# Performance work log

Measured on AMD Instinct MI355X. Metric: run time of the kernel, lower is better.

Reference implementation:

```python
import jax, jax.numpy as jnp
import numpy as np

DIM = 1536
HEADS = 12
HD = DIM // HEADS           # 128
C = HD // 2                 # 64 rotary pairs per head
B = 1
F_, H_, W_ = 16, 16, 16
S = F_ * H_ * W_            # 4096
MAXPOS = 1024
EPS = 1e-6
SPLITS = (C - 2 * (C // 3), C // 3, C // 3)  # (22, 21, 21)


def setup_inputs() -> dict:
    key = jax.random.key(0)
    ks = jax.random.split(key, 8)
    std = 0.02
    x = jax.random.normal(ks[0], (B, S, DIM), jnp.float32)
    seq_lens = jnp.full((B,), S, dtype=jnp.int32)
    grid_sizes = jnp.tile(jnp.array([[F_, H_, W_]], jnp.int32), (B, 1))
    # rotary angle table: per split, theta_j = pos / 10000^(j/size)
    angs = []
    pos = jnp.arange(MAXPOS, dtype=jnp.float32)
    for sz in SPLITS:
        inv = 1.0 / (10000.0 ** (jnp.arange(sz, dtype=jnp.float32) / sz))
        angs.append(jnp.outer(pos, inv))
    freqs = jnp.concatenate(angs, axis=1)  # [MAXPOS, C]
    return {
        "x": x,
        "seq_lens": seq_lens,
        "grid_sizes": grid_sizes,
        "freqs": freqs,
        "wq": jax.random.normal(ks[1], (DIM, DIM), jnp.float32) * std,
        "bq": jnp.zeros((DIM,), jnp.float32),
        "wk": jax.random.normal(ks[2], (DIM, DIM), jnp.float32) * std,
        "bk": jnp.zeros((DIM,), jnp.float32),
        "wv": jax.random.normal(ks[3], (DIM, DIM), jnp.float32) * std,
        "bv": jnp.zeros((DIM,), jnp.float32),
        "wo": jax.random.normal(ks[4], (DIM, DIM), jnp.float32) * std,
        "bo": jnp.zeros((DIM,), jnp.float32),
        "gq": jnp.ones((DIM,), jnp.float32),
        "gk": jnp.ones((DIM,), jnp.float32),
    }


def _rms_norm(x, g):
    # x * rsqrt(mean(x^2) + eps) * g  (WanRMSNorm)
    var = jnp.mean(jnp.square(x), axis=-1, keepdims=True)
    return x * jax.lax.rsqrt(var + EPS) * g


def _rope(x, freqs, f, h, w):
    # x: [b, s, n, hd]; freqs: [MAXPOS, C] angles; grid (f,h,w), s = f*h*w
    fa = freqs[:f, : SPLITS[0]]
    ha = freqs[:h, SPLITS[0] : SPLITS[0] + SPLITS[1]]
    wa = freqs[:w, SPLITS[0] + SPLITS[1] :]
    ang = jnp.concatenate(
        [
            jnp.broadcast_to(fa[:, None, None, :], (f, h, w, SPLITS[0])),
            jnp.broadcast_to(ha[None, :, None, :], (f, h, w, SPLITS[1])),
            jnp.broadcast_to(wa[None, None, :, :], (f, h, w, SPLITS[2])),
        ],
        axis=-1,
    ).reshape(f * h * w, 1, C)  # [s, 1, C] broadcasts over heads
    cos, sin = jnp.cos(ang), jnp.sin(ang)
    xr = x[..., 0::2]  # real parts of complex pairs
    xi = x[..., 1::2]  # imag parts
    out_r = xr * cos - xi * sin
    out_i = xr * sin + xi * cos
    return jnp.stack([out_r, out_i], axis=-1).reshape(x.shape)


def reference(x, seq_lens, grid_sizes, freqs, wq, bq, wk, bk, wv, bv, wo, bo, gq, gk):
    b, s = x.shape[:2]
    q = _rms_norm(x @ wq.T + bq, gq).reshape(b, s, HEADS, HD)
    k = _rms_norm(x @ wk.T + bk, gk).reshape(b, s, HEADS, HD)
    v = (x @ wv.T + bv).reshape(b, s, HEADS, HD)
    # all samples share the same grid (static for jit)
    q = _rope(q, freqs, F_, H_, W_)
    k = _rope(k, freqs, F_, H_, W_)
    scale = 1.0 / np.sqrt(HD)
    scores = jnp.einsum("bqnd,bknd->bnqk", q, k) * scale  # [b, n, s, s]
    k_pos = jnp.arange(s)
    mask = k_pos[None, None, None, :] < seq_lens[:, None, None, None]
    scores = scores + jnp.where(mask, 0.0, -1e9)
    attn = jax.nn.softmax(scores, axis=-1)
    out = jnp.einsum("bnqk,bknd->bqnd", attn, v).reshape(b, s, DIM)
    return out @ wo.T + bo
```

## Files before the change

kernel.cpp:

```cpp
#include <hip/hip_runtime.h>
#include <hip/hip_bf16.h>

#define DIM   1536
#define HEADS 12
#define HD    128
#define SEQ   4096
#define QSCALE 0.08838834764831845f
#define LOG2E 1.44269504088896f

typedef __attribute__((ext_vector_type(8))) short short8;
typedef __attribute__((ext_vector_type(4))) float f32x4;
typedef __attribute__((ext_vector_type(16))) float f32x16;

__device__ __forceinline__ unsigned short f2bf(float f) {
    __hip_bfloat16 h = __float2bfloat16(f);
    return *reinterpret_cast<unsigned short*>(&h);
}
__device__ __forceinline__ float bf2f(unsigned short u) {
    return __uint_as_float(((unsigned int)u) << 16);
}
__device__ __forceinline__ void async_cp16(void* lds, const void* g) {
    __builtin_amdgcn_global_load_lds(
        (const __attribute__((address_space(1))) unsigned int*)g,
        (__attribute__((address_space(3))) unsigned int*)lds, 16, 0, 0);
}

__global__ __launch_bounds__(256) void convert_bf16(
    const float* __restrict__ src, __hip_bfloat16* __restrict__ dst, int n8)
{
    const int i = blockIdx.x * 256 + threadIdx.x;
    if (i >= n8) return;
    const float4 a = *reinterpret_cast<const float4*>(src + (size_t)i * 8);
    const float4 b = *reinterpret_cast<const float4*>(src + (size_t)i * 8 + 4);
    uint4 o;
    o.x = (unsigned int)f2bf(a.x) | ((unsigned int)f2bf(a.y) << 16);
    o.y = (unsigned int)f2bf(a.z) | ((unsigned int)f2bf(a.w) << 16);
    o.z = (unsigned int)f2bf(b.x) | ((unsigned int)f2bf(b.y) << 16);
    o.w = (unsigned int)f2bf(b.z) | ((unsigned int)f2bf(b.w) << 16);
    *reinterpret_cast<uint4*>(dst + (size_t)i * 8) = o;
}

__global__ __launch_bounds__(256) void gemm_qkv(
    const __hip_bfloat16* __restrict__ xb,
    const __hip_bfloat16* __restrict__ wqb, const float* __restrict__ bq,
    const __hip_bfloat16* __restrict__ wkb, const float* __restrict__ bk,
    const __hip_bfloat16* __restrict__ wvb, const float* __restrict__ bv,
    __hip_bfloat16* __restrict__ yq, __hip_bfloat16* __restrict__ yk,
    __hip_bfloat16* __restrict__ vrow)
{
    __shared__ __align__(16) short As[128][32];
    __shared__ __align__(16) short Bs[128][32];
    const int z  = blockIdx.z;
    const __hip_bfloat16* W = (z == 0) ? wqb : (z == 1) ? wkb : wvb;
    const float* bias = (z == 0) ? bq : (z == 1) ? bk : bv;
    __hip_bfloat16* outp = (z == 0) ? yq : (z == 1) ? yk : vrow;
    const int bm0 = blockIdx.x * 128;
    const int bn0 = blockIdx.y * 128;
    const int tid  = threadIdx.x;
    const int lane = tid & 63;
    const int wid  = tid >> 6;
    const int wm = (wid >> 1) * 64;
    const int wn = (wid & 1)  * 64;
    const int fr = lane & 15;
    const int fc = (lane >> 4) * 8;
    const int srow = tid >> 2;
    const int scol = (tid & 3) * 8;

    f32x4 acc[4][4] = {};

    for (int kt = 0; kt < DIM; kt += 32) {
        #pragma unroll
        for (int i = 0; i < 2; i++) {
            async_cp16(&As[i * 64 + ((tid >> 6) << 4)][0],
                       xb + (size_t)(bm0 + i * 64 + srow) * DIM + kt + scol);
            async_cp16(&Bs[i * 64 + ((tid >> 6) << 4)][0],
                       W + (size_t)(bn0 + i * 64 + srow) * DIM + kt + scol);
        }
        __syncthreads();
        short8 af[4], bf8[4];
        #pragma unroll
        for (int m = 0; m < 4; m++) af[m]  = *reinterpret_cast<const short8*>(&As[wm + m * 16 + fr][fc]);
        #pragma unroll
        for (int n = 0; n < 4; n++) bf8[n] = *reinterpret_cast<const short8*>(&Bs[wn + n * 16 + fr][fc]);
        #pragma unroll
        for (int m = 0; m < 4; m++)
            #pragma unroll
            for (int n = 0; n < 4; n++)
                acc[m][n] = __builtin_amdgcn_mfma_f32_16x16x32_bf16(af[m], bf8[n], acc[m][n], 0, 0, 0);
        __syncthreads();
    }

    const int crow0 = bm0 + wm + (lane >> 4) * 4;
    const int ccol0 = bn0 + wn + fr;
    #pragma unroll
    for (int n = 0; n < 4; n++) {
        const int col = ccol0 + n * 16;
        const float bb = bias[col];
        #pragma unroll
        for (int m = 0; m < 4; m++)
            #pragma unroll
            for (int r = 0; r < 4; r++)
                outp[(size_t)(crow0 + m * 16 + r) * DIM + col] =
                    __float2bfloat16(acc[m][n][r] + bb);
    }
}

__global__ __launch_bounds__(256) void rmsnorm_rope(
    __hip_bfloat16* __restrict__ yq, __hip_bfloat16* __restrict__ yk,
    const float* __restrict__ gq, const float* __restrict__ gk,
    const float* __restrict__ freqs)
{
    const int s = blockIdx.x;
    const int z = blockIdx.y;
    __hip_bfloat16* y = z ? yk : yq;
    const float* g = z ? gk : gq;
    const int t = threadIdx.x;

    float xr[3], xi[3];
    float ss = 0.f;
    #pragma unroll
    for (int i = 0; i < 3; i++) {
        const int p = t + i * 256;
        const unsigned int uu = *reinterpret_cast<const unsigned int*>(&y[(size_t)s * DIM + 2 * p]);
        xr[i] = bf2f((unsigned short)(uu & 0xffffu));
        xi[i] = bf2f((unsigned short)(uu >> 16));
        ss += xr[i] * xr[i] + xi[i] * xi[i];
    }
    #pragma unroll
    for (int m = 1; m < 64; m <<= 1) ss += __shfl_xor(ss, m, 64);
    __shared__ float red[4];
    if ((t & 63) == 0) red[t >> 6] = ss;
    __syncthreads();
    const float sum = red[0] + red[1] + red[2] + red[3];
    const float rs = rsqrtf(sum * (1.0f / DIM) + 1e-6f);
    const int f = s >> 8, hh = (s >> 4) & 15, ww = s & 15;
    const float osc = z ? 1.0f : QSCALE;
    #pragma unroll
    for (int i = 0; i < 3; i++) {
        const int p = t + i * 256;
        const int cc = p & 63;
        const int pos = (cc < 22) ? f : (cc < 43) ? hh : ww;
        const float ang = freqs[pos * 64 + cc];
        float sn, cs;
        sincosf(ang, &sn, &cs);
        const float a = xr[i] * rs * g[2 * p];
        const float b = xi[i] * rs * g[2 * p + 1];
        const unsigned int pk = (unsigned int)f2bf((a * cs - b * sn) * osc)
                              | ((unsigned int)f2bf((a * sn + b * cs) * osc) << 16);
        *reinterpret_cast<unsigned int*>(&y[(size_t)s * DIM + 2 * p]) = pk;
    }
}

__global__ __launch_bounds__(256) void transpose_v(
    const __hip_bfloat16* __restrict__ vrow,
    __hip_bfloat16* __restrict__ vT)
{
    __shared__ __align__(16) short tile[64][72];
    const int s0 = blockIdx.x * 64;
    const int c0 = blockIdx.y * 64;
    const int t = threadIdx.x;
    #pragma unroll
    for (int i = 0; i < 2; i++) {
        const int ch = t + i * 256;
        const int r = ch >> 3, cc = (ch & 7) * 8;
        *reinterpret_cast<int4*>(&tile[r][cc]) =
            *reinterpret_cast<const int4*>(&vrow[(size_t)(s0 + r) * DIM + c0 + cc]);
    }
    __syncthreads();
    #pragma unroll
    for (int i = 0; i < 2; i++) {
        const int ch = t + i * 256;
        const int c = ch & 63, sc = (ch >> 6) * 8;
        unsigned int w0 = (unsigned short)tile[sc + 0][c] | ((unsigned int)(unsigned short)tile[sc + 1][c] << 16);
        unsigned int w1 = (unsigned short)tile[sc + 2][c] | ((unsigned int)(unsigned short)tile[sc + 3][c] << 16);
        unsigned int w2 = (unsigned short)tile[sc + 4][c] | ((unsigned int)(unsigned short)tile[sc + 5][c] << 16);
        unsigned int w3 = (unsigned short)tile[sc + 6][c] | ((unsigned int)(unsigned short)tile[sc + 7][c] << 16);
        int4 val;
        val.x = (int)w0; val.y = (int)w1; val.z = (int)w2; val.w = (int)w3;
        *reinterpret_cast<int4*>(&vT[(size_t)(c0 + c) * SEQ + s0 + sc]) = val;
    }
}

__global__ __launch_bounds__(256, 2) void flash_attn(
    const __hip_bfloat16* __restrict__ qb,
    const __hip_bfloat16* __restrict__ kb,
    const __hip_bfloat16* __restrict__ vT,
    const int* __restrict__ seq_lens,
    __hip_bfloat16* __restrict__ attno)
{
    __shared__ __align__(16) short Ks[2][64][128];
    __shared__ __align__(16) short Vs[3][128][64];
    const int qt = blockIdx.x;
    const int h  = blockIdx.y;
    const int tid = threadIdx.x;
    const int lane = tid & 63;
    const int w = tid >> 6;
    const int q5 = lane & 31;
    const int hi = lane >> 5;
    const int seqlen = seq_lens[0];
    const int swz = (lane & 7) << 4;
    const int NT = SEQ / 64;

    short8 qf[8];
    const int qrow = qt * 128 + w * 32 + q5;
    #pragma unroll
    for (int s = 0; s < 8; s++)
        qf[s] = *reinterpret_cast<const short8*>(&qb[(size_t)qrow * DIM + h * HD + s * 16 + hi * 8]);

    f32x16 oacc[4] = {};
    float m = -1e30f, l = 0.f;
    unsigned int Wp[2][4][2];
    f32x16 saccA[2], saccB[2];

    const int kROW = w * 4 + (lane >> 4);
    const int kCOL = ((lane & 15) ^ (kROW & 7)) * 8;
    const int vROW = w * 8 + (lane >> 3);
    const int vCOL = (((lane & 7) ^ (vROW & 7))) * 8;

    auto stageK = [&](int tile, int slot) {
        #pragma unroll
        for (int i = 0; i < 4; i++)
            async_cp16(&Ks[slot][i * 16 + w * 4][0],
                       kb + (size_t)(tile * 64 + i * 16 + kROW) * DIM + h * HD + kCOL);
    };
    auto stageV = [&](int tile, int slot) {
        #pragma unroll
        for (int i = 0; i < 4; i++)
            async_cp16(&Vs[slot][i * 32 + vROW][0],
                       vT + ((size_t)h * HD + i * 32 + vROW) * SEQ + tile * 64 + vCOL);
    };
    auto qk = [&](int slot, f32x16* S) {
        const char* Kp = (const char*)&Ks[slot][0][0];
        S[0] = (f32x16){};
        S[1] = (f32x16){};
        __builtin_amdgcn_s_setprio(1);
        #pragma unroll
        for (int s = 0; s < 8; s++) {
            #pragma unroll
            for (int kbk = 0; kbk < 2; kbk++) {
                short8 kf = *reinterpret_cast<const short8*>(
                    Kp + (kbk * 32 + q5) * 256 + ((s * 32 + hi * 16) ^ swz));
                S[kbk] = __builtin_amdgcn_mfma_f32_32x32x16_bf16(kf, qf[s], S[kbk], 0, 0, 0);
            }
        }
        __builtin_amdgcn_s_setprio(0);
    };
    auto pv = [&](int slot) {
        const char* Vp = (const char*)&Vs[slot][0][0];
        #pragma unroll
        for (int ks = 0; ks < 4; ks++) {
            const int kbk = ks >> 1;
            const int te = (ks & 1) * 2, to = te + 1;
            const int a0 = (int)Wp[kbk][te][0], a1 = (int)Wp[kbk][te][1];
            const int b0 = (int)Wp[kbk][to][0], b1 = (int)Wp[kbk][to][1];
            const int xa0 = __shfl_xor(a0, 32, 64);
            const int xa1 = __shfl_xor(a1, 32, 64);
            const int xb0 = __shfl_xor(b0, 32, 64);
            const int xb1 = __shfl_xor(b1, 32, 64);
            int4 pwv;
            pwv.x = hi ? xb0 : a0;
            pwv.y = hi ? xb1 : a1;
            pwv.z = hi ? b0  : xa0;
            pwv.w = hi ? b1  : xa1;
            const short8 pf = __builtin_bit_cast(short8, pwv);
            __builtin_amdgcn_s_setprio(1);
            #pragma unroll
            for (int cb = 0; cb < 4; cb++) {
                short8 vf = *reinterpret_cast<const short8*>(
                    Vp + (cb * 32 + q5) * 128 + ((ks * 32 + hi * 16) ^ swz));
                oacc[cb] = __builtin_amdgcn_mfma_f32_32x32x16_bf16(vf, pf, oacc[cb], 0, 0, 0);
            }
            __builtin_amdgcn_s_setprio(0);
        }
    };
    auto softmax_step = [&](int tt, f32x16* S) {
        const int kbase = tt * 64;
        float tmax = -1e30f;
        if (kbase + 64 <= seqlen) {
            #pragma unroll
            for (int kbk = 0; kbk < 2; kbk++)
                #pragma unroll
                for (int r = 0; r < 16; r++) tmax = fmaxf(tmax, S[kbk][r]);
        } else {
            #pragma unroll
            for (int kbk = 0; kbk < 2; kbk++)
                #pragma unroll
                for (int r = 0; r < 16; r++) {
                    const int key = kbase + kbk * 32 + (r & 3) + 8 * (r >> 2) + 4 * hi;
                    const float sv = (key < seqlen) ? S[kbk][r] : -1e30f;
                    S[kbk][r] = sv;
                    tmax = fmaxf(tmax, sv);
                }
        }
        tmax = fmaxf(tmax, __shfl_xor(tmax, 32, 64));
        if (!__all(tmax <= m + 8.0f)) {
            const float mn = fmaxf(m, tmax);
            const float alpha = exp2f((m - mn) * LOG2E);
            m = mn;
            l *= alpha;
            #pragma unroll
            for (int cb = 0; cb < 4; cb++)
                #pragma unroll
                for (int r = 0; r < 16; r++) oacc[cb][r] *= alpha;
        }
        float ps = 0.f;
        #pragma unroll
        for (int kbk = 0; kbk < 2; kbk++)
            #pragma unroll
            for (int r = 0; r < 16; r++) {
                const float p = exp2f((S[kbk][r] - m) * LOG2E);
                S[kbk][r] = p;
                ps += p;
            }
        ps += __shfl_xor(ps, 32, 64);
        l += ps;
        #pragma unroll
        for (int kbk = 0; kbk < 2; kbk++)
            #pragma unroll
            for (int tq = 0; tq < 4; tq++) {
                Wp[kbk][tq][0] = (unsigned int)f2bf(S[kbk][4 * tq + 0])
                               | ((unsigned int)f2bf(S[kbk][4 * tq + 1]) << 16);
                Wp[kbk][tq][1] = (unsigned int)f2bf(S[kbk][4 * tq + 2])
                               | ((unsigned int)f2bf(S[kbk][4 * tq + 3]) << 16);
            }
    };
    auto iter_body = [&](int t, f32x16* Scur, f32x16* Snxt) {
        __syncthreads();
        stageV(t + 1, (t + 1) % 3);
        if (t + 2 < NT) stageK(t + 2, t & 1);
        qk((t + 1) & 1, Snxt);
        pv((t - 1) % 3);
        softmax_step(t, Scur);
    };

    stageK(0, 0); stageV(0, 0);
    __syncthreads();
    stageK(1, 1); stageV(1, 1);
    qk(0, saccA);
    __syncthreads();
    stageK(2, 0);
    qk(1, saccB);
    softmax_step(0, saccA);

    for (int t = 1; t + 1 <= NT - 2; t += 2) {
        iter_body(t,     saccB, saccA);
        iter_body(t + 1, saccA, saccB);
    }

    __syncthreads();
    pv((NT - 2) % 3);
    softmax_step(NT - 1, saccB);
    pv((NT - 1) % 3);

    const float inv_l = 1.f / l;
    const size_t obase = (size_t)qrow * DIM + h * HD;
    #pragma unroll
    for (int cb = 0; cb < 4; cb++) {
        #pragma unroll
        for (int tq = 0; tq < 4; tq++) {
            uint2 pko;
            pko.x = (unsigned int)f2bf(oacc[cb][4 * tq + 0] * inv_l)
                  | ((unsigned int)f2bf(oacc[cb][4 * tq + 1] * inv_l) << 16);
            pko.y = (unsigned int)f2bf(oacc[cb][4 * tq + 2] * inv_l)
                  | ((unsigned int)f2bf(oacc[cb][4 * tq + 3] * inv_l) << 16);
            *reinterpret_cast<uint2*>(&attno[obase + cb * 32 + 8 * tq + 4 * hi]) = pko;
        }
    }
}

__global__ __launch_bounds__(256) void gemm_out(
    const __hip_bfloat16* __restrict__ A,
    const __hip_bfloat16* __restrict__ W,
    const float* __restrict__ bias,
    float* __restrict__ outp)
{
    __shared__ __align__(16) short As[128][32];
    __shared__ __align__(16) short Bs[128][32];
    const int bm0 = blockIdx.x * 128;
    const int bn0 = blockIdx.y * 128;
    const int tid = threadIdx.x;
    const int lane = tid & 63;
    const int wid = tid >> 6;
    const int wm = (wid >> 1) * 64;
    const int wn = (wid & 1) * 64;
    const int fr = lane & 15;
    const int fc = (lane >> 4) * 8;
    const int srow = tid >> 2;
    const int scol = (tid & 3) * 8;

    f32x4 acc[4][4] = {};

    for (int kt = 0; kt < DIM; kt += 32) {
        #pragma unroll
        for (int i = 0; i < 2; i++) {
            async_cp16(&As[i * 64 + ((tid >> 6) << 4)][0],
                       A + (size_t)(bm0 + i * 64 + srow) * DIM + kt + scol);
            async_cp16(&Bs[i * 64 + ((tid >> 6) << 4)][0],
                       W + (size_t)(bn0 + i * 64 + srow) * DIM + kt + scol);
        }
        __syncthreads();
        short8 af[4], bf8[4];
        #pragma unroll
        for (int m = 0; m < 4; m++) af[m]  = *reinterpret_cast<const short8*>(&As[wm + m * 16 + fr][fc]);
        #pragma unroll
        for (int n = 0; n < 4; n++) bf8[n] = *reinterpret_cast<const short8*>(&Bs[wn + n * 16 + fr][fc]);
        #pragma unroll
        for (int m = 0; m < 4; m++)
            #pragma unroll
            for (int n = 0; n < 4; n++)
                acc[m][n] = __builtin_amdgcn_mfma_f32_16x16x32_bf16(af[m], bf8[n], acc[m][n], 0, 0, 0);
        __syncthreads();
    }

    const int crow0 = bm0 + wm + (lane >> 4) * 4;
    const int ccol0 = bn0 + wn + fr;
    #pragma unroll
    for (int n = 0; n < 4; n++) {
        const int col = ccol0 + n * 16;
        const float bb = bias[col];
        #pragma unroll
        for (int m = 0; m < 4; m++)
            #pragma unroll
            for (int r = 0; r < 4; r++)
                outp[(size_t)(crow0 + m * 16 + r) * DIM + col] = acc[m][n][r] + bb;
    }
}

extern "C" void kernel_launch(void* const* d_in, const int* in_sizes, int n_in,
                              void* d_out, int out_size, void* d_ws, size_t ws_size,
                              hipStream_t stream)
{
    const float* x        = (const float*)d_in[0];
    const int*   seq_lens = (const int*)d_in[1];
    const float* freqs    = (const float*)d_in[3];
    const float* wq = (const float*)d_in[4];
    const float* bq = (const float*)d_in[5];
    const float* wk = (const float*)d_in[6];
    const float* bk = (const float*)d_in[7];
    const float* wv = (const float*)d_in[8];
    const float* bv = (const float*)d_in[9];
    const float* wo = (const float*)d_in[10];
    const float* bo = (const float*)d_in[11];
    const float* gq = (const float*)d_in[12];
    const float* gk = (const float*)d_in[13];
    float* out = (float*)d_out;

    char* ws = (char*)d_ws;
    __hip_bfloat16* yq    = (__hip_bfloat16*)(ws);
    __hip_bfloat16* yk    = (__hip_bfloat16*)(ws + 12582912);
    __hip_bfloat16* vrow  = (__hip_bfloat16*)(ws + 25165824);
    __hip_bfloat16* vT    = (__hip_bfloat16*)(ws + 37748736);
    __hip_bfloat16* attno = (__hip_bfloat16*)(ws + 25165824);
    __hip_bfloat16* xb    = (__hip_bfloat16*)(ws + 37748736);
    __hip_bfloat16* wob   = (__hip_bfloat16*)(ws);
    __hip_bfloat16* wqb   = (__hip_bfloat16*)d_out;
    __hip_bfloat16* wkb   = wqb + 2359296;
    __hip_bfloat16* wvb   = wkb + 2359296;

    dim3 blk(256);
    convert_bf16<<<dim3(3072), blk, 0, stream>>>(x,  xb,  786432);
    convert_bf16<<<dim3(1152), blk, 0, stream>>>(wq, wqb, 294912);
    convert_bf16<<<dim3(1152), blk, 0, stream>>>(wk, wkb, 294912);
    convert_bf16<<<dim3(1152), blk, 0, stream>>>(wv, wvb, 294912);
    gemm_qkv    <<<dim3(32, 12, 3), blk, 0, stream>>>(xb, wqb, bq, wkb, bk, wvb, bv, yq, yk, vrow);
    rmsnorm_rope<<<dim3(4096, 2),   blk, 0, stream>>>(yq, yk, gq, gk, freqs);
    transpose_v <<<dim3(64, 24),    blk, 0, stream>>>(vrow, vT);
    flash_attn  <<<dim3(32, 12),    blk, 0, stream>>>(yq, yk, vT, seq_lens, attno);
    convert_bf16<<<dim3(1152), blk, 0, stream>>>(wo, wob, 294912);
    gemm_out    <<<dim3(32, 12),    blk, 0, stream>>>(attno, wob, bo, out);
}
```

Baseline: 328.9 us.

## Merge conversion and norm/transpose launches, restructure flash attention pipeline

Folds the four fp32-to-bf16 conversions into one launch, and merges RMSNorm+RoPE with the V transpose into one launch, so fewer kernels are launched. Inside flash attention, the two-stage software pipeline that kept two score tiles in flight is replaced by a simpler loop. Each iteration now computes QK for the current tile, then PV for the previous tile, then softmax. The softmax uses tree reductions and an FMA-form exponent, and the PV operand lane shuffles move into the softmax step. This cuts live registers and launch overhead, but gives up some overlap between QK and softmax.

```diff
diff --git a/kernel.cpp b/kernel.cpp
--- a/kernel.cpp
+++ b/kernel.cpp
@@ -38,6 +38,30 @@
     o.z = (unsigned int)f2bf(b.x) | ((unsigned int)f2bf(b.y) << 16);
     o.w = (unsigned int)f2bf(b.z) | ((unsigned int)f2bf(b.w) << 16);
     *reinterpret_cast<uint4*>(dst + (size_t)i * 8) = o;
+}
+
+__global__ __launch_bounds__(256) void convert_all(
+    const float* __restrict__ x,  const float* __restrict__ wq,
+    const float* __restrict__ wk, const float* __restrict__ wv,
+    __hip_bfloat16* __restrict__ xb,  __hip_bfloat16* __restrict__ wqb,
+    __hip_bfloat16* __restrict__ wkb, __hip_bfloat16* __restrict__ wvb)
+{
+    const int i = blockIdx.x * 256 + threadIdx.x;
+    const float* src;
+    __hip_bfloat16* dst;
+    int off;
+    if (i < 786432)            { src = x;  dst = xb;  off = i; }
+    else if (i < 1081344)      { src = wq; dst = wqb; off = i - 786432; }
+    else if (i < 1376256)      { src = wk; dst = wkb; off = i - 1081344; }
+    else                       { src = wv; dst = wvb; off = i - 1376256; }
+    const float4 a = *reinterpret_cast<const float4*>(src + (size_t)off * 8);
+    const float4 b = *reinterpret_cast<const float4*>(src + (size_t)off * 8 + 4);
+    uint4 o;
+    o.x = (unsigned int)f2bf(a.x) | ((unsigned int)f2bf(a.y) << 16);
+    o.y = (unsigned int)f2bf(a.z) | ((unsigned int)f2bf(a.w) << 16);
+    o.z = (unsigned int)f2bf(b.x) | ((unsigned int)f2bf(b.y) << 16);
+    o.w = (unsigned int)f2bf(b.z) | ((unsigned int)f2bf(b.w) << 16);
+    *reinterpret_cast<uint4*>(dst + (size_t)off * 8) = o;
 }
 
 __global__ __launch_bounds__(256) void gemm_qkv(
@@ -105,79 +129,79 @@
     }
 }
 
-__global__ __launch_bounds__(256) void rmsnorm_rope(
+__global__ __launch_bounds__(256) void norm_rope_transpose(
     __hip_bfloat16* __restrict__ yq, __hip_bfloat16* __restrict__ yk,
     const float* __restrict__ gq, const float* __restrict__ gk,
-    const float* __restrict__ freqs)
-{
-    const int s = blockIdx.x;
-    const int z = blockIdx.y;
-    __hip_bfloat16* y = z ? yk : yq;
-    const float* g = z ? gk : gq;
+    const float* __restrict__ freqs,
+    const __hip_bfloat16* __restrict__ vrow, __hip_bfloat16* __restrict__ vT)
+{
+    __shared__ float red[4];
+    __shared__ __align__(16) short tile[64][72];
+    const int b = blockIdx.x;
     const int t = threadIdx.x;
 
-    float xr[3], xi[3];
-    float ss = 0.f;
-    #pragma unroll
-    for (int i = 0; i < 3; i++) {
-        const int p = t + i * 256;
-        const unsigned int uu = *reinterpret_cast<const unsigned int*>(&y[(size_t)s * DIM + 2 * p]);
-        xr[i] = bf2f((unsigned short)(uu & 0xffffu));
-        xi[i] = bf2f((unsigned short)(uu >> 16));
-        ss += xr[i] * xr[i] + xi[i] * xi[i];
-    }
-    #pragma unroll
-    for (int m = 1; m < 64; m <<= 1) ss += __shfl_xor(ss, m, 64);
-    __shared__ float red[4];
-    if ((t & 63) == 0) red[t >> 6] = ss;
-    __syncthreads();
-    const float sum = red[0] + red[1] + red[2] + red[3];
-    const float rs = rsqrtf(sum * (1.0f / DIM) + 1e-6f);
-    const int f = s >> 8, hh = (s >> 4) & 15, ww = s & 15;
-    const float osc = z ? 1.0f : QSCALE;
-    #pragma unroll
-    for (int i = 0; i < 3; i++) {
-        const int p = t + i * 256;
-        const int cc = p & 63;
-        const int pos = (cc < 22) ? f : (cc < 43) ? hh : ww;
-        const float ang = freqs[pos * 64 + cc];
-        float sn, cs;
-        sincosf(ang, &sn, &cs);
-        const float a = xr[i] * rs * g[2 * p];
-        const float b = xi[i] * rs * g[2 * p + 1];
-        const unsigned int pk = (unsigned int)f2bf((a * cs - b * sn) * osc)
-                              | ((unsigned int)f2bf((a * sn + b * cs) * osc) << 16);
-        *reinterpret_cast<unsigned int*>(&y[(size_t)s * DIM + 2 * p]) = pk;
-    }
-}
-
-__global__ __launch_bounds__(256) void transpose_v(
-    const __hip_bfloat16* __restrict__ vrow,
-    __hip_bfloat16* __restrict__ vT)
-{
-    __shared__ __align__(16) short tile[64][72];
-    const int s0 = blockIdx.x * 64;
-    const int c0 = blockIdx.y * 64;
-    const int t = threadIdx.x;
-    #pragma unroll
-    for (int i = 0; i < 2; i++) {
-        const int ch = t + i * 256;
-        const int r = ch >> 3, cc = (ch & 7) * 8;
-        *reinterpret_cast<int4*>(&tile[r][cc]) =
-            *reinterpret_cast<const int4*>(&vrow[(size_t)(s0 + r) * DIM + c0 + cc]);
-    }
-    __syncthreads();
-    #pragma unroll
-    for (int i = 0; i < 2; i++) {
-        const int ch = t + i * 256;
-        const int c = ch & 63, sc = (ch >> 6) * 8;
-        unsigned int w0 = (unsigned short)tile[sc + 0][c] | ((unsigned int)(unsigned short)tile[sc + 1][c] << 16);
-        unsigned int w1 = (unsigned short)tile[sc + 2][c] | ((unsigned int)(unsigned short)tile[sc + 3][c] << 16);
-        unsigned int w2 = (unsigned short)tile[sc + 4][c] | ((unsigned int)(unsigned short)tile[sc + 5][c] << 16);
-        unsigned int w3 = (unsigned short)tile[sc + 6][c] | ((unsigned int)(unsigned short)tile[sc + 7][c] << 16);
-        int4 val;
-        val.x = (int)w0; val.y = (int)w1; val.z = (int)w2; val.w = (int)w3;
-        *reinterpret_cast<int4*>(&vT[(size_t)(c0 + c) * SEQ + s0 + sc]) = val;
+    if (b < 8192) {
+        const int s = b >> 1;
+        const int z = b & 1;
+        __hip_bfloat16* y = z ? yk : yq;
+        const float* g = z ? gk : gq;
+
+        float xr[3], xi[3];
+        float ss = 0.f;
+        #pragma unroll
+        for (int i = 0; i < 3; i++) {
+            const int p = t + i * 256;
+            const unsigned int uu = *reinterpret_cast<const unsigned int*>(&y[(size_t)s * DIM + 2 * p]);
+            xr[i] = bf2f((unsigned short)(uu & 0xffffu));
+            xi[i] = bf2f((unsigned short)(uu >> 16));
+            ss += xr[i] * xr[i] + xi[i] * xi[i];
+        }
+        #pragma unroll
+        for (int m = 1; m < 64; m <<= 1) ss += __shfl_xor(ss, m, 64);
+        if ((t & 63) == 0) red[t >> 6] = ss;
+        __syncthreads();
+        const float sum = red[0] + red[1] + red[2] + red[3];
+        const float rs = rsqrtf(sum * (1.0f / DIM) + 1e-6f);
+        const int f = s >> 8, hh = (s >> 4) & 15, ww = s & 15;
+        const float osc = z ? 1.0f : QSCALE;
+        #pragma unroll
+        for (int i = 0; i < 3; i++) {
+            const int p = t + i * 256;
+            const int cc = p & 63;
+            const int pos = (cc < 22) ? f : (cc < 43) ? hh : ww;
+            const float ang = freqs[pos * 64 + cc];
+            float sn, cs;
+            sincosf(ang, &sn, &cs);
+            const float a = xr[i] * rs * g[2 * p];
+            const float bb = xi[i] * rs * g[2 * p + 1];
+            const unsigned int pk = (unsigned int)f2bf((a * cs - bb * sn) * osc)
+                                  | ((unsigned int)f2bf((a * sn + bb * cs) * osc) << 16);
+            *reinterpret_cast<unsigned int*>(&y[(size_t)s * DIM + 2 * p]) = pk;
+        }
+    } else {
+        const int tb = b - 8192;
+        const int s0 = (tb & 63) * 64;
+        const int c0 = (tb >> 6) * 64;
+        #pragma unroll
+        for (int i = 0; i < 2; i++) {
+            const int ch = t + i * 256;
+            const int r = ch >> 3, cc = (ch & 7) * 8;
+            *reinterpret_cast<int4*>(&tile[r][cc]) =
+                *reinterpret_cast<const int4*>(&vrow[(size_t)(s0 + r) * DIM + c0 + cc]);
+        }
+        __syncthreads();
+        #pragma unroll
+        for (int i = 0; i < 2; i++) {
+            const int ch = t + i * 256;
+            const int c = ch & 63, sc = (ch >> 6) * 8;
+            unsigned int w0 = (unsigned short)tile[sc + 0][c] | ((unsigned int)(unsigned short)tile[sc + 1][c] << 16);
+            unsigned int w1 = (unsigned short)tile[sc + 2][c] | ((unsigned int)(unsigned short)tile[sc + 3][c] << 16);
+            unsigned int w2 = (unsigned short)tile[sc + 4][c] | ((unsigned int)(unsigned short)tile[sc + 5][c] << 16);
+            unsigned int w3 = (unsigned short)tile[sc + 6][c] | ((unsigned int)(unsigned short)tile[sc + 7][c] << 16);
+            int4 val;
+            val.x = (int)w0; val.y = (int)w1; val.z = (int)w2; val.w = (int)w3;
+            *reinterpret_cast<int4*>(&vT[(size_t)(c0 + c) * SEQ + s0 + sc]) = val;
+        }
     }
 }
 
@@ -209,8 +233,7 @@
 
     f32x16 oacc[4] = {};
     float m = -1e30f, l = 0.f;
-    unsigned int Wp[2][4][2];
-    f32x16 saccA[2], saccB[2];
+    unsigned int WpG[4][4];
 
     const int kROW = w * 4 + (lane >> 4);
     const int kCOL = ((lane & 15) ^ (kROW & 7)) * 8;
@@ -229,58 +252,34 @@
             async_cp16(&Vs[slot][i * 32 + vROW][0],
                        vT + ((size_t)h * HD + i * 32 + vROW) * SEQ + tile * 64 + vCOL);
     };
-    auto qk = [&](int slot, f32x16* S) {
-        const char* Kp = (const char*)&Ks[slot][0][0];
-        S[0] = (f32x16){};
-        S[1] = (f32x16){};
-        __builtin_amdgcn_s_setprio(1);
-        #pragma unroll
-        for (int s = 0; s < 8; s++) {
-            #pragma unroll
-            for (int kbk = 0; kbk < 2; kbk++) {
-                short8 kf = *reinterpret_cast<const short8*>(
-                    Kp + (kbk * 32 + q5) * 256 + ((s * 32 + hi * 16) ^ swz));
-                S[kbk] = __builtin_amdgcn_mfma_f32_32x32x16_bf16(kf, qf[s], S[kbk], 0, 0, 0);
-            }
-        }
-        __builtin_amdgcn_s_setprio(0);
-    };
     auto pv = [&](int slot) {
         const char* Vp = (const char*)&Vs[slot][0][0];
+        __builtin_amdgcn_s_setprio(1);
         #pragma unroll
         for (int ks = 0; ks < 4; ks++) {
-            const int kbk = ks >> 1;
-            const int te = (ks & 1) * 2, to = te + 1;
-            const int a0 = (int)Wp[kbk][te][0], a1 = (int)Wp[kbk][te][1];
-            const int b0 = (int)Wp[kbk][to][0], b1 = (int)Wp[kbk][to][1];
-            const int xa0 = __shfl_xor(a0, 32, 64);
-            const int xa1 = __shfl_xor(a1, 32, 64);
-            const int xb0 = __shfl_xor(b0, 32, 64);
-            const int xb1 = __shfl_xor(b1, 32, 64);
             int4 pwv;
-            pwv.x = hi ? xb0 : a0;
-            pwv.y = hi ? xb1 : a1;
-            pwv.z = hi ? b0  : xa0;
-            pwv.w = hi ? b1  : xa1;
+            pwv.x = (int)WpG[ks][0];
+            pwv.y = (int)WpG[ks][1];
+            pwv.z = (int)WpG[ks][2];
+            pwv.w = (int)WpG[ks][3];
             const short8 pf = __builtin_bit_cast(short8, pwv);
-            __builtin_amdgcn_s_setprio(1);
             #pragma unroll
             for (int cb = 0; cb < 4; cb++) {
                 short8 vf = *reinterpret_cast<const short8*>(
                     Vp + (cb * 32 + q5) * 128 + ((ks * 32 + hi * 16) ^ swz));
                 oacc[cb] = __builtin_amdgcn_mfma_f32_32x32x16_bf16(vf, pf, oacc[cb], 0, 0, 0);
             }
-            __builtin_amdgcn_s_setprio(0);
-        }
+        }
+        __builtin_amdgcn_s_setprio(0);
     };
-    auto softmax_step = [&](int tt, f32x16* S) {
+    auto softmax_pack = [&](int tt, f32x16* S) {
         const int kbase = tt * 64;
-        float tmax = -1e30f;
+        float v[32];
         if (kbase + 64 <= seqlen) {
             #pragma unroll
             for (int kbk = 0; kbk < 2; kbk++)
                 #pragma unroll
-                for (int r = 0; r < 16; r++) tmax = fmaxf(tmax, S[kbk][r]);
+                for (int r = 0; r < 16; r++) v[kbk * 16 + r] = S[kbk][r];
         } else {
             #pragma unroll
             for (int kbk = 0; kbk < 2; kbk++)
@@ -289,10 +288,15 @@
                     const int key = kbase + kbk * 32 + (r & 3) + 8 * (r >> 2) + 4 * hi;
                     const float sv = (key < seqlen) ? S[kbk][r] : -1e30f;
                     S[kbk][r] = sv;
-                    tmax = fmaxf(tmax, sv);
+                    v[kbk * 16 + r] = sv;
                 }
         }
-        tmax = fmaxf(tmax, __shfl_xor(tmax, 32, 64));
+        #pragma unroll
+        for (int st = 16; st >= 1; st >>= 1)
+            #pragma unroll
+            for (int i = 0; i < st; i++) v[i] = fmaxf(v[i], v[i + st]);
+        float tmax = fmaxf(v[0], __shfl_xor(v[0], 32, 64));
+
         if (!__all(tmax <= m + 8.0f)) {
             const float mn = fmaxf(m, tmax);
             const float alpha = exp2f((m - mn) * LOG2E);
@@ -303,54 +307,86 @@
                 #pragma unroll
                 for (int r = 0; r < 16; r++) oacc[cb][r] *= alpha;
         }
-        float ps = 0.f;
+        const float nmL = -m * LOG2E;
         #pragma unroll
         for (int kbk = 0; kbk < 2; kbk++)
             #pragma unroll
             for (int r = 0; r < 16; r++) {
-                const float p = exp2f((S[kbk][r] - m) * LOG2E);
+                const float p = exp2f(fmaf(S[kbk][r], LOG2E, nmL));
                 S[kbk][r] = p;
-                ps += p;
+                v[kbk * 16 + r] = p;
             }
-        ps += __shfl_xor(ps, 32, 64);
-        l += ps;
+        #pragma unroll
+        for (int st = 16; st >= 1; st >>= 1)
+            #pragma unroll
+            for (int i = 0; i < st; i++) v[i] += v[i + st];
+        l += v[0] + __shfl_xor(v[0], 32, 64);
+
+        unsigned int Wl[2][4][2];
         #pragma unroll
         for (int kbk = 0; kbk < 2; kbk++)
             #pragma unroll
             for (int tq = 0; tq < 4; tq++) {
-                Wp[kbk][tq][0] = (unsigned int)f2bf(S[kbk][4 * tq + 0])
+                Wl[kbk][tq][0] = (unsigned int)f2bf(S[kbk][4 * tq + 0])
                                | ((unsigned int)f2bf(S[kbk][4 * tq + 1]) << 16);
-                Wp[kbk][tq][1] = (unsigned int)f2bf(S[kbk][4 * tq + 2])
+                Wl[kbk][tq][1] = (unsigned int)f2bf(S[kbk][4 * tq + 2])
                                | ((unsigned int)f2bf(S[kbk][4 * tq + 3]) << 16);
             }
+        #pragma unroll
+        for (int ks = 0; ks < 4; ks++) {
+            const int kbk = ks >> 1;
+            const int te = (ks & 1) * 2, to = te + 1;
+            const int a0 = (int)Wl[kbk][te][0], a1 = (int)Wl[kbk][te][1];
+            const int b0 = (int)Wl[kbk][to][0], b1 = (int)Wl[kbk][to][1];
+            const int xa0 = __shfl_xor(a0, 32, 64);
+            const int xa1 = __shfl_xor(a1, 32, 64);
+            const int xb0 = __shfl_xor(b0, 32, 64);
+            const int xb1 = __shfl_xor(b1, 32, 64);
+            WpG[ks][0] = (unsigned int)(hi ? xb0 : a0);
+            WpG[ks][1] = (unsigned int)(hi ? xb1 : a1);
+            WpG[ks][2] = (unsigned int)(hi ? b0  : xa0);
+            WpG[ks][3] = (unsigned int)(hi ? b1  : xa1);
+        }
     };
-    auto iter_body = [&](int t, f32x16* Scur, f32x16* Snxt) {
-        __syncthreads();
-        stageV(t + 1, (t + 1) % 3);
-        if (t + 2 < NT) stageK(t + 2, t & 1);
-        qk((t + 1) & 1, Snxt);
-        pv((t - 1) % 3);
-        softmax_step(t, Scur);
+    auto qk = [&](int slot, f32x16* S) {
+        const char* Kp = (const char*)&Ks[slot][0][0];
+        __builtin_amdgcn_s_setprio(1);
+        #pragma unroll
+        for (int s = 0; s < 8; s++)
+            #pragma unroll
+            for (int kbk = 0; kbk < 2; kbk++) {
+                short8 kf = *reinterpret_cast<const short8*>(
+                    Kp + (kbk * 32 + q5) * 256 + ((s * 32 + hi * 16) ^ swz));
+                S[kbk] = __builtin_amdgcn_mfma_f32_32x32x16_bf16(kf, qf[s], S[kbk], 0, 0, 0);
+            }
+        __builtin_amdgcn_s_setprio(0);
     };
 
     stageK(0, 0); stageV(0, 0);
     __syncthreads();
     stageK(1, 1); stageV(1, 1);
-    qk(0, saccA);
-    __syncthreads();
-    stageK(2, 0);
-    qk(1, saccB);
-    softmax_step(0, saccA);
-
-    for (int t = 1; t + 1 <= NT - 2; t += 2) {
-        iter_body(t,     saccB, saccA);
-        iter_body(t + 1, saccA, saccB);
-    }
-
-    __syncthreads();
-    pv((NT - 2) % 3);
-    softmax_step(NT - 1, saccB);
-    pv((NT - 1) % 3);
+    {
+        f32x16 sacc[2] = {};
+        qk(0, sacc);
+        softmax_pack(0, sacc);
+    }
+
+    int vprev = 0, vnext = 2;
+    for (int t = 1; t < NT; t++) {
+        __syncthreads();
+        if (t + 1 < NT) {
+            stageK(t + 1, (t + 1) & 1);
+            stageV(t + 1, vnext);
+        }
+        f32x16 sacc[2] = {};
+        qk(t & 1, sacc);
+        pv(vprev);
+        softmax_pack(t, sacc);
+        vprev = (vprev == 2) ? 0 : vprev + 1;
+        vnext = (vnext == 2) ? 0 : vnext + 1;
+    }
+
+    pv(vprev);
 
     const float inv_l = 1.f / l;
     const size_t obase = (size_t)qrow * DIM + h * HD;
@@ -458,14 +494,10 @@
     __hip_bfloat16* wvb   = wkb + 2359296;
 
     dim3 blk(256);
-    convert_bf16<<<dim3(3072), blk, 0, stream>>>(x,  xb,  786432);
-    convert_bf16<<<dim3(1152), blk, 0, stream>>>(wq, wqb, 294912);
-    convert_bf16<<<dim3(1152), blk, 0, stream>>>(wk, wkb, 294912);
-    convert_bf16<<<dim3(1152), blk, 0, stream>>>(wv, wvb, 294912);
-    gemm_qkv    <<<dim3(32, 12, 3), blk, 0, stream>>>(xb, wqb, bq, wkb, bk, wvb, bv, yq, yk, vrow);
-    rmsnorm_rope<<<dim3(4096, 2),   blk, 0, stream>>>(yq, yk, gq, gk, freqs);
-    transpose_v <<<dim3(64, 24),    blk, 0, stream>>>(vrow, vT);
-    flash_attn  <<<dim3(32, 12),    blk, 0, stream>>>(yq, yk, vT, seq_lens, attno);
-    convert_bf16<<<dim3(1152), blk, 0, stream>>>(wo, wob, 294912);
-    gemm_out    <<<dim3(32, 12),    blk, 0, stream>>>(attno, wob, bo, out);
-}
+    convert_all        <<<dim3(6528), blk, 0, stream>>>(x, wq, wk, wv, xb, wqb, wkb, wvb);
+    gemm_qkv           <<<dim3(32, 12, 3), blk, 0, stream>>>(xb, wqb, bq, wkb, bk, wvb, bv, yq, yk, vrow);
+    norm_rope_transpose<<<dim3(9728), blk, 0, stream>>>(yq, yk, gq, gk, freqs, vrow, vT);
+    flash_attn         <<<dim3(32, 12), blk, 0, stream>>>(yq, yk, vT, seq_lens, attno);
+    convert_bf16       <<<dim3(1152), blk, 0, stream>>>(wo, wob, 294912);
+    gemm_out           <<<dim3(32, 12), blk, 0, stream>>>(attno, wob, bo, out);
+}
```

Result: no change. 324.0 us (-1.5%).
